# Performance work log

Measured on AMD Instinct MI355X. Metric: run time of the kernel, lower is better.

## Reference

```python
import jax, jax.numpy as jnp
import numpy as np

B, N, D, H, C = 4, 512, 128, 128, 3


def setup_inputs() -> dict:
    key = jax.random.key(0)
    k1, k2, k3, k4, k5 = jax.random.split(key, 5)
    s1 = 1.0 / np.sqrt(2 * D)  # torch Linear default init scale (uniform bound); randn is fine for a numerics baseline
    s2 = 1.0 / np.sqrt(H)
    return {
        "h_dense": jax.random.normal(k1, (B, N, D), dtype=jnp.float32),
        "W1": jax.random.normal(k2, (H, 2 * D), dtype=jnp.float32) * s1,
        "b1": jax.random.normal(k3, (H,), dtype=jnp.float32) * s1,
        "W2": jax.random.normal(k4, (C, H), dtype=jnp.float32) * s2,
        "b2": jax.random.normal(k5, (C,), dtype=jnp.float32) * s2,
    }


def reference(h_dense, W1, b1, W2, b2):
    # Linear(concat(h_src, h_dst)) == h_src @ W1[:, :D].T + h_dst @ W1[:, D:].T + b1
    # which avoids materializing the (B, N, N, 2D) concat tensor (same math).
    d = h_dense.shape[-1]
    a = jnp.einsum("bnd,hd->bnh", h_dense, W1[:, :d])  # src projection (B, N, H)
    b = jnp.einsum("bnd,hd->bnh", h_dense, W1[:, d:])  # dst projection (B, N, H)
    pre = a[:, :, None, :] + b[:, None, :, :] + b1      # (B, N, N, H)
    act = jax.nn.silu(pre)
    logits = jnp.einsum("bijh,ch->bijc", act, W2) + b2  # (B, N, N, C)
    # symmetrize over the pair axes (dropout is identity in eval mode)
    return (logits + jnp.swapaxes(logits, 1, 2)) * 0.5
```

## Files before the change

### kernel.cpp

```cpp
#include <hip/hip_runtime.h>
#include <hip/hip_fp16.h>

#define B_ 4
#define N_ 512
#define D_ 128
#define H_ 128
#define C_ 3

#define NEG_LOG2E   (-1.4426950408889634f)
#define NEG_HALF_LN2 (-0.34657359027997264f)
#define ROWP 136

typedef _Float16 half8  __attribute__((ext_vector_type(8)));
typedef _Float16 half4v __attribute__((ext_vector_type(4)));

__device__ __forceinline__ float exp2_fast(float x) {
    return __builtin_amdgcn_exp2f(x);
}

__global__ __launch_bounds__(256) void proj_gemm(
    const float* __restrict__ hd, const float* __restrict__ W1,
    const float* __restrict__ b1, _Float16* __restrict__ At, _Float16* __restrict__ Bt)
{
    __shared__ float hsT[64][36];
    __shared__ float wt [64][68];
    const int m0      = blockIdx.x * 32;
    const int by      = blockIdx.y;
    const int halfSel = by >> 1;
    const int wrow0   = (by & 1) * 64;

    const int t  = threadIdx.x;
    const int r  = t >> 4, c4 = t & 15;
    const int tx = t & 15, ty = t >> 4;

    float acc[2][4] = {};

    for (int kc = 0; kc < 2; ++kc) {
        if (kc) __syncthreads();
        #pragma unroll
        for (int i = 0; i < 2; ++i) {
            const int m = r + 16 * i;
            float4 v = *(const float4*)&hd[(m0 + m) * D_ + kc * 64 + 4 * c4];
            hsT[4 * c4 + 0][m] = v.x; hsT[4 * c4 + 1][m] = v.y;
            hsT[4 * c4 + 2][m] = v.z; hsT[4 * c4 + 3][m] = v.w;
        }
        #pragma unroll
        for (int i = 0; i < 4; ++i) {
            const int o = r + 16 * i;
            float4 v = *(const float4*)&W1[(wrow0 + o) * (2 * D_) + halfSel * D_ + kc * 64 + 4 * c4];
            wt[4 * c4 + 0][o] = v.x; wt[4 * c4 + 1][o] = v.y;
            wt[4 * c4 + 2][o] = v.z; wt[4 * c4 + 3][o] = v.w;
        }
        __syncthreads();
        #pragma unroll 8
        for (int k = 0; k < 64; ++k) {
            float2 a  = *(const float2*)&hsT[k][2 * ty];
            float4 bv = *(const float4*)&wt [k][4 * tx];
            acc[0][0] = fmaf(a.x, bv.x, acc[0][0]); acc[0][1] = fmaf(a.x, bv.y, acc[0][1]);
            acc[0][2] = fmaf(a.x, bv.z, acc[0][2]); acc[0][3] = fmaf(a.x, bv.w, acc[0][3]);
            acc[1][0] = fmaf(a.y, bv.x, acc[1][0]); acc[1][1] = fmaf(a.y, bv.y, acc[1][1]);
            acc[1][2] = fmaf(a.y, bv.z, acc[1][2]); acc[1][3] = fmaf(a.y, bv.w, acc[1][3]);
        }
    }

    _Float16* dst = halfSel ? Bt : At;
    const int ocol = wrow0 + 4 * tx;
    float4 bias = make_float4(0.f, 0.f, 0.f, 0.f);
    if (!halfSel) bias = *(const float4*)&b1[ocol];
    #pragma unroll
    for (int i = 0; i < 2; ++i) {
        half4v o;
        o[0] = (_Float16)((acc[i][0] + bias.x) * NEG_LOG2E);
        o[1] = (_Float16)((acc[i][1] + bias.y) * NEG_LOG2E);
        o[2] = (_Float16)((acc[i][2] + bias.z) * NEG_LOG2E);
        o[3] = (_Float16)((acc[i][3] + bias.w) * NEG_LOG2E);
        *(half4v*)&dst[(m0 + 2 * ty + i) * H_ + ocol] = o;
    }
}

__global__ __launch_bounds__(256, 8) void pair_kernel(
    const _Float16* __restrict__ At, const _Float16* __restrict__ Bt,
    const float* __restrict__ W2, const float* __restrict__ b2,
    float* __restrict__ out)
{
    __shared__ __align__(16) _Float16 AI[16 * ROWP], AJ[16 * ROWP];
    __shared__ __align__(16) _Float16 BI[16 * ROWP], BJ[16 * ROWP];
    const int T = N_ / 16;
    int tp = blockIdx.x;
    const int b = blockIdx.y;
    int I = 0;
    while (tp >= T - I) { tp -= T - I; ++I; }
    const int J = I + tp;

    const int tid = threadIdx.x;
    {
        const int r = tid >> 4, c = (tid & 15) * 8;
        const half8* sAI = (const half8*)(At + (b * N_ + I * 16) * H_);
        const half8* sAJ = (const half8*)(At + (b * N_ + J * 16) * H_);
        const half8* sBI = (const half8*)(Bt + (b * N_ + I * 16) * H_);
        const half8* sBJ = (const half8*)(Bt + (b * N_ + J * 16) * H_);
        *(half8*)&AI[r * ROWP + c] = sAI[tid];
        *(half8*)&AJ[r * ROWP + c] = sAJ[tid];
        *(half8*)&BI[r * ROWP + c] = sBI[tid];
        *(half8*)&BJ[r * ROWP + c] = sBJ[tid];
    }
    __syncthreads();

    const int ti = tid >> 4, tj = tid & 15;
    float acc0 = 0.f, acc1 = 0.f, acc2 = 0.f;

    #pragma unroll 4
    for (int h8 = 0; h8 < H_ / 8; ++h8) {
        const int hb = h8 * 8;
        half8 ai8 = *(const half8*)&AI[ti * ROWP + hb];
        half8 bj8 = *(const half8*)&BJ[tj * ROWP + hb];
        half8 aj8 = *(const half8*)&AJ[tj * ROWP + hb];
        half8 bi8 = *(const half8*)&BI[ti * ROWP + hb];
        float4 w0a = *(const float4*)&W2[hb],          w0b = *(const float4*)&W2[hb + 4];
        float4 w1a = *(const float4*)&W2[H_ + hb],     w1b = *(const float4*)&W2[H_ + hb + 4];
        float4 w2a = *(const float4*)&W2[2 * H_ + hb], w2b = *(const float4*)&W2[2 * H_ + hb + 4];
        const float w0[8] = {w0a.x, w0a.y, w0a.z, w0a.w, w0b.x, w0b.y, w0b.z, w0b.w};
        const float w1[8] = {w1a.x, w1a.y, w1a.z, w1a.w, w1b.x, w1b.y, w1b.z, w1b.w};
        const float w2[8] = {w2a.x, w2a.y, w2a.z, w2a.w, w2b.x, w2b.y, w2b.z, w2b.w};

        #pragma unroll
        for (int e = 0; e < 8; ++e) {
            const float y1 = (float)(ai8[e] + bj8[e]);
            const float y2 = (float)(aj8[e] + bi8[e]);
            const float d1 = 1.0f + exp2_fast(y1);
            const float d2 = 1.0f + exp2_fast(y2);
            const float rr = __builtin_amdgcn_rcpf(d1 * d2);
            const float s  = fmaf(y2, d1, y1 * d2) * rr;
            acc0 = fmaf(s, w0[e], acc0);
            acc1 = fmaf(s, w1[e], acc1);
            acc2 = fmaf(s, w2[e], acc2);
        }
    }

    const float o0 = fmaf(NEG_HALF_LN2, acc0, b2[0]);
    const float o1 = fmaf(NEG_HALF_LN2, acc1, b2[1]);
    const float o2 = fmaf(NEG_HALF_LN2, acc2, b2[2]);
    const int i = I * 16 + ti, j = J * 16 + tj;
    float* p1 = out + ((size_t)(b * N_ + i) * N_ + j) * C_;
    float* p2 = out + ((size_t)(b * N_ + j) * N_ + i) * C_;
    p1[0] = o0; p1[1] = o1; p1[2] = o2;
    p2[0] = o0; p2[1] = o1; p2[2] = o2;
}

extern "C" void kernel_launch(void* const* d_in, const int* in_sizes, int n_in,
                              void* d_out, int out_size, void* d_ws, size_t ws_size,
                              hipStream_t stream) {
    const float* hd = (const float*)d_in[0];
    const float* W1 = (const float*)d_in[1];
    const float* b1 = (const float*)d_in[2];
    const float* W2 = (const float*)d_in[3];
    const float* b2 = (const float*)d_in[4];
    float* out = (float*)d_out;

    _Float16* At = (_Float16*)d_ws;
    _Float16* Bt = At + B_ * N_ * H_;

    proj_gemm<<<dim3((B_ * N_) / 32, 4), dim3(256), 0, stream>>>(hd, W1, b1, At, Bt);

    const int T = N_ / 16;
    pair_kernel<<<dim3(T * (T + 1) / 2, B_), dim3(256), 0, stream>>>(At, Bt, W2, b2, out);
}
```

Before: 48.08 us.

## Precompute exp2 of projections and compute pair SiLU in packed fp16

The projection kernel now also writes exp2 of each projected value, so the pair kernel gets exp(a+b) as a product exp(a)*exp(b) instead of calling exp per pair element. The symmetric sigmoid numerator and denominator are computed in packed half2 arithmetic, leaving only a reciprocal per element in fp32. The pair kernel is reorganised into 64-thread blocks where each thread handles one j and four i rows, reading directly from global memory (no LDS staging) over a triangular tile enumeration. The workspace grows to four fp16 buffers, and fp16 products of exponentials risk overflow or precision loss for large inputs.

Result: slower. 62.24 us (+29.5%).

```diff
diff --git a/kernel.cpp b/kernel.cpp
--- a/kernel.cpp
+++ b/kernel.cpp
@@ -9,10 +9,10 @@
 
 #define NEG_LOG2E   (-1.4426950408889634f)
 #define NEG_HALF_LN2 (-0.34657359027997264f)
-#define ROWP 136
 
 typedef _Float16 half8  __attribute__((ext_vector_type(8)));
 typedef _Float16 half4v __attribute__((ext_vector_type(4)));
+typedef _Float16 half2v __attribute__((ext_vector_type(2)));
 
 __device__ __forceinline__ float exp2_fast(float x) {
     return __builtin_amdgcn_exp2f(x);
@@ -20,7 +20,9 @@
 
 __global__ __launch_bounds__(256) void proj_gemm(
     const float* __restrict__ hd, const float* __restrict__ W1,
-    const float* __restrict__ b1, _Float16* __restrict__ At, _Float16* __restrict__ Bt)
+    const float* __restrict__ b1,
+    _Float16* __restrict__ At,  _Float16* __restrict__ Bt,
+    _Float16* __restrict__ EAt, _Float16* __restrict__ EBt)
 {
     __shared__ float hsT[64][36];
     __shared__ float wt [64][68];
@@ -63,59 +65,61 @@
         }
     }
 
-    _Float16* dst = halfSel ? Bt : At;
+    _Float16* dst  = halfSel ? Bt  : At;
+    _Float16* edst = halfSel ? EBt : EAt;
     const int ocol = wrow0 + 4 * tx;
-    float4 bias = make_float4(0.f, 0.f, 0.f, 0.f);
-    if (!halfSel) bias = *(const float4*)&b1[ocol];
+    float biasv[4] = {0.f, 0.f, 0.f, 0.f};
+    if (!halfSel) {
+        float4 bb = *(const float4*)&b1[ocol];
+        biasv[0] = bb.x; biasv[1] = bb.y; biasv[2] = bb.z; biasv[3] = bb.w;
+    }
     #pragma unroll
     for (int i = 0; i < 2; ++i) {
-        half4v o;
-        o[0] = (_Float16)((acc[i][0] + bias.x) * NEG_LOG2E);
-        o[1] = (_Float16)((acc[i][1] + bias.y) * NEG_LOG2E);
-        o[2] = (_Float16)((acc[i][2] + bias.z) * NEG_LOG2E);
-        o[3] = (_Float16)((acc[i][3] + bias.w) * NEG_LOG2E);
-        *(half4v*)&dst[(m0 + 2 * ty + i) * H_ + ocol] = o;
+        half4v o, ee;
+        #pragma unroll
+        for (int k = 0; k < 4; ++k) {
+            o[k]  = (_Float16)((acc[i][k] + biasv[k]) * NEG_LOG2E);
+            ee[k] = (_Float16)exp2_fast((float)o[k]);
+        }
+        const size_t off = (size_t)(m0 + 2 * ty + i) * H_ + ocol;
+        *(half4v*)&dst[off]  = o;
+        *(half4v*)&edst[off] = ee;
     }
 }
 
-__global__ __launch_bounds__(256, 8) void pair_kernel(
-    const _Float16* __restrict__ At, const _Float16* __restrict__ Bt,
+__global__ __launch_bounds__(64, 4) void pair_kernel(
+    const _Float16* __restrict__ At,  const _Float16* __restrict__ Bt,
+    const _Float16* __restrict__ EAt, const _Float16* __restrict__ EBt,
     const float* __restrict__ W2, const float* __restrict__ b2,
     float* __restrict__ out)
 {
-    __shared__ __align__(16) _Float16 AI[16 * ROWP], AJ[16 * ROWP];
-    __shared__ __align__(16) _Float16 BI[16 * ROWP], BJ[16 * ROWP];
-    const int T = N_ / 16;
-    int tp = blockIdx.x;
     const int b = blockIdx.y;
-    int I = 0;
-    while (tp >= T - I) { tp -= T - I; ++I; }
-    const int J = I + tp;
+    int x = blockIdx.x;
+    int jt = 0;
+    for (;;) {
+        int cnt = 16 * (jt + 1); if (cnt > 128) cnt = 128;
+        if (x < cnt) break;
+        x -= cnt; ++jt;
+    }
+    const int i0 = x * 4;
+    const int j  = jt * 64 + (int)threadIdx.x;
 
-    const int tid = threadIdx.x;
-    {
-        const int r = tid >> 4, c = (tid & 15) * 8;
-        const half8* sAI = (const half8*)(At + (b * N_ + I * 16) * H_);
-        const half8* sAJ = (const half8*)(At + (b * N_ + J * 16) * H_);
-        const half8* sBI = (const half8*)(Bt + (b * N_ + I * 16) * H_);
-        const half8* sBJ = (const half8*)(Bt + (b * N_ + J * 16) * H_);
-        *(half8*)&AI[r * ROWP + c] = sAI[tid];
-        *(half8*)&AJ[r * ROWP + c] = sAJ[tid];
-        *(half8*)&BI[r * ROWP + c] = sBI[tid];
-        *(half8*)&BJ[r * ROWP + c] = sBJ[tid];
-    }
-    __syncthreads();
+    const size_t jbase = ((size_t)(b * N_) + j)  * H_;
+    const size_t ibase = ((size_t)(b * N_) + i0) * H_;
 
-    const int ti = tid >> 4, tj = tid & 15;
-    float acc0 = 0.f, acc1 = 0.f, acc2 = 0.f;
+    float acc[4][3] = {};
 
-    #pragma unroll 4
-    for (int h8 = 0; h8 < H_ / 8; ++h8) {
-        const int hb = h8 * 8;
-        half8 ai8 = *(const half8*)&AI[ti * ROWP + hb];
-        half8 bj8 = *(const half8*)&BJ[tj * ROWP + hb];
-        half8 aj8 = *(const half8*)&AJ[tj * ROWP + hb];
-        half8 bi8 = *(const half8*)&BI[ti * ROWP + hb];
+    for (int ch = 0; ch < 16; ++ch) {
+        const int hb = ch * 8;
+        const half8 yAj = *(const half8*)&At [jbase + hb];
+        const half8 yBj = *(const half8*)&Bt [jbase + hb];
+        const half8 eAj = *(const half8*)&EAt[jbase + hb];
+        const half8 eBj = *(const half8*)&EBt[jbase + hb];
+        const half2v* yAj2p = (const half2v*)&yAj;
+        const half2v* yBj2p = (const half2v*)&yBj;
+        const half2v* eAj2p = (const half2v*)&eAj;
+        const half2v* eBj2p = (const half2v*)&eBj;
+
         float4 w0a = *(const float4*)&W2[hb],          w0b = *(const float4*)&W2[hb + 4];
         float4 w1a = *(const float4*)&W2[H_ + hb],     w1b = *(const float4*)&W2[H_ + hb + 4];
         float4 w2a = *(const float4*)&W2[2 * H_ + hb], w2b = *(const float4*)&W2[2 * H_ + hb + 4];
@@ -124,27 +128,54 @@
         const float w2[8] = {w2a.x, w2a.y, w2a.z, w2a.w, w2b.x, w2b.y, w2b.z, w2b.w};
 
         #pragma unroll
-        for (int e = 0; e < 8; ++e) {
-            const float y1 = (float)(ai8[e] + bj8[e]);
-            const float y2 = (float)(aj8[e] + bi8[e]);
-            const float d1 = 1.0f + exp2_fast(y1);
-            const float d2 = 1.0f + exp2_fast(y2);
-            const float rr = __builtin_amdgcn_rcpf(d1 * d2);
-            const float s  = fmaf(y2, d1, y1 * d2) * rr;
-            acc0 = fmaf(s, w0[e], acc0);
-            acc1 = fmaf(s, w1[e], acc1);
-            acc2 = fmaf(s, w2[e], acc2);
+        for (int ii = 0; ii < 4; ++ii) {
+            const size_t ir = ibase + (size_t)ii * H_ + hb;
+            const half8 yAi = *(const half8*)&At [ir];
+            const half8 yBi = *(const half8*)&Bt [ir];
+            const half8 eAi = *(const half8*)&EAt[ir];
+            const half8 eBi = *(const half8*)&EBt[ir];
+            const half2v* yAi2p = (const half2v*)&yAi;
+            const half2v* yBi2p = (const half2v*)&yBi;
+            const half2v* eAi2p = (const half2v*)&eAi;
+            const half2v* eBi2p = (const half2v*)&eBi;
+
+            #pragma unroll
+            for (int q = 0; q < 4; ++q) {
+                half2v y1 = yAi2p[q] + yBj2p[q];
+                half2v y2 = yAj2p[q] + yBi2p[q];
+                half2v e1 = eAi2p[q] * eBj2p[q];
+                half2v e2 = eAj2p[q] * eBi2p[q];
+                half2v d1 = e1 + (_Float16)1.0f;
+                half2v d2 = e2 + (_Float16)1.0f;
+                half2v pp  = d1 * d2;
+                half2v num = y1 * d2 + y2 * d1;
+
+                #pragma unroll
+                for (int e = 0; e < 2; ++e) {
+                    const float s = (float)num[e] * __builtin_amdgcn_rcpf((float)pp[e]);
+                    const int hh = 2 * q + e;
+                    acc[ii][0] = fmaf(s, w0[hh], acc[ii][0]);
+                    acc[ii][1] = fmaf(s, w1[hh], acc[ii][1]);
+                    acc[ii][2] = fmaf(s, w2[hh], acc[ii][2]);
+                }
+            }
         }
     }
 
-    const float o0 = fmaf(NEG_HALF_LN2, acc0, b2[0]);
-    const float o1 = fmaf(NEG_HALF_LN2, acc1, b2[1]);
-    const float o2 = fmaf(NEG_HALF_LN2, acc2, b2[2]);
-    const int i = I * 16 + ti, j = J * 16 + tj;
-    float* p1 = out + ((size_t)(b * N_ + i) * N_ + j) * C_;
-    float* p2 = out + ((size_t)(b * N_ + j) * N_ + i) * C_;
-    p1[0] = o0; p1[1] = o1; p1[2] = o2;
-    p2[0] = o0; p2[1] = o1; p2[2] = o2;
+    const float b20 = b2[0], b21 = b2[1], b22 = b2[2];
+    #pragma unroll
+    for (int ii = 0; ii < 4; ++ii) {
+        const int i = i0 + ii;
+        if (j >= i) {
+            const float o0 = fmaf(NEG_HALF_LN2, acc[ii][0], b20);
+            const float o1 = fmaf(NEG_HALF_LN2, acc[ii][1], b21);
+            const float o2 = fmaf(NEG_HALF_LN2, acc[ii][2], b22);
+            float* p1 = out + ((size_t)(b * N_ + i) * N_ + j) * C_;
+            float* p2 = out + ((size_t)(b * N_ + j) * N_ + i) * C_;
+            p1[0] = o0; p1[1] = o1; p1[2] = o2;
+            p2[0] = o0; p2[1] = o1; p2[2] = o2;
+        }
+    }
 }
 
 extern "C" void kernel_launch(void* const* d_in, const int* in_sizes, int n_in,
@@ -157,11 +188,12 @@
     const float* b2 = (const float*)d_in[4];
     float* out = (float*)d_out;
 
-    _Float16* At = (_Float16*)d_ws;
-    _Float16* Bt = At + B_ * N_ * H_;
+    _Float16* At  = (_Float16*)d_ws;
+    _Float16* Bt  = At  + B_ * N_ * H_;
+    _Float16* EAt = Bt  + B_ * N_ * H_;
+    _Float16* EBt = EAt + B_ * N_ * H_;
 
-    proj_gemm<<<dim3((B_ * N_) / 32, 4), dim3(256), 0, stream>>>(hd, W1, b1, At, Bt);
+    proj_gemm<<<dim3((B_ * N_) / 32, 4), dim3(256), 0, stream>>>(hd, W1, b1, At, Bt, EAt, EBt);
 
-    const int T = N_ / 16;
-    pair_kernel<<<dim3(T * (T + 1) / 2, B_), dim3(256), 0, stream>>>(At, Bt, W2, b2, out);
+    pair_kernel<<<dim3(576, B_), dim3(64), 0, stream>>>(At, Bt, EAt, EBt, W2, b2, out);
 }
```

## Precompute exp2 of projections and factor pairwise exp into fp16 products

Applied to the files above, without the earlier changes.

The projection kernel now also writes exp2 of each projected value, so the pair kernel can form exp(a+b) as a product of two precomputed exponentials instead of calling exp2 per pair element. The sigmoid numerator and denominator are computed in packed fp16 vector arithmetic, and only one reciprocal per element stays in fp32. The pair kernel stages only the J tile in shared memory and reads the I-side rows directly from global memory, and its occupancy hint drops from 8 to 4 blocks. This doubles workspace traffic and risks fp16 overflow or precision loss in the exponential products.

New measurement: 57.12 us. +18.8%, slower.

```diff
diff --git a/kernel.cpp b/kernel.cpp
--- a/kernel.cpp
+++ b/kernel.cpp
@@ -9,7 +9,7 @@
 
 #define NEG_LOG2E   (-1.4426950408889634f)
 #define NEG_HALF_LN2 (-0.34657359027997264f)
-#define ROWP 136
+#define TPAD 132
 
 typedef _Float16 half8  __attribute__((ext_vector_type(8)));
 typedef _Float16 half4v __attribute__((ext_vector_type(4)));
@@ -20,7 +20,9 @@
 
 __global__ __launch_bounds__(256) void proj_gemm(
     const float* __restrict__ hd, const float* __restrict__ W1,
-    const float* __restrict__ b1, _Float16* __restrict__ At, _Float16* __restrict__ Bt)
+    const float* __restrict__ b1,
+    _Float16* __restrict__ At,  _Float16* __restrict__ Bt,
+    _Float16* __restrict__ EAt, _Float16* __restrict__ EBt)
 {
     __shared__ float hsT[64][36];
     __shared__ float wt [64][68];
@@ -63,59 +65,82 @@
         }
     }
 
-    _Float16* dst = halfSel ? Bt : At;
+    _Float16* dst  = halfSel ? Bt  : At;
+    _Float16* edst = halfSel ? EBt : EAt;
     const int ocol = wrow0 + 4 * tx;
-    float4 bias = make_float4(0.f, 0.f, 0.f, 0.f);
-    if (!halfSel) bias = *(const float4*)&b1[ocol];
+    float biasv[4] = {0.f, 0.f, 0.f, 0.f};
+    if (!halfSel) {
+        float4 bb = *(const float4*)&b1[ocol];
+        biasv[0] = bb.x; biasv[1] = bb.y; biasv[2] = bb.z; biasv[3] = bb.w;
+    }
     #pragma unroll
     for (int i = 0; i < 2; ++i) {
-        half4v o;
-        o[0] = (_Float16)((acc[i][0] + bias.x) * NEG_LOG2E);
-        o[1] = (_Float16)((acc[i][1] + bias.y) * NEG_LOG2E);
-        o[2] = (_Float16)((acc[i][2] + bias.z) * NEG_LOG2E);
-        o[3] = (_Float16)((acc[i][3] + bias.w) * NEG_LOG2E);
-        *(half4v*)&dst[(m0 + 2 * ty + i) * H_ + ocol] = o;
+        half4v o, ee;
+        #pragma unroll
+        for (int k = 0; k < 4; ++k) {
+            o[k]  = (_Float16)((acc[i][k] + biasv[k]) * NEG_LOG2E);
+            ee[k] = (_Float16)exp2_fast((float)o[k]);
+        }
+        const size_t off = (size_t)(m0 + 2 * ty + i) * H_ + ocol;
+        *(half4v*)&dst[off]  = o;
+        *(half4v*)&edst[off] = ee;
     }
 }
 
-__global__ __launch_bounds__(256, 8) void pair_kernel(
-    const _Float16* __restrict__ At, const _Float16* __restrict__ Bt,
+__global__ __launch_bounds__(256, 4) void pair_kernel(
+    const _Float16* __restrict__ At,  const _Float16* __restrict__ Bt,
+    const _Float16* __restrict__ EAt, const _Float16* __restrict__ EBt,
     const float* __restrict__ W2, const float* __restrict__ b2,
     float* __restrict__ out)
 {
-    __shared__ __align__(16) _Float16 AI[16 * ROWP], AJ[16 * ROWP];
-    __shared__ __align__(16) _Float16 BI[16 * ROWP], BJ[16 * ROWP];
-    const int T = N_ / 16;
+    __shared__ __align__(16) _Float16 jt[4][16 * TPAD];
+    const int b = blockIdx.y;
     int tp = blockIdx.x;
-    const int b = blockIdx.y;
     int I = 0;
-    while (tp >= T - I) { tp -= T - I; ++I; }
+    while (tp >= 32 - I) { tp -= 32 - I; ++I; }
     const int J = I + tp;
 
     const int tid = threadIdx.x;
-    {
-        const int r = tid >> 4, c = (tid & 15) * 8;
-        const half8* sAI = (const half8*)(At + (b * N_ + I * 16) * H_);
-        const half8* sAJ = (const half8*)(At + (b * N_ + J * 16) * H_);
-        const half8* sBI = (const half8*)(Bt + (b * N_ + I * 16) * H_);
-        const half8* sBJ = (const half8*)(Bt + (b * N_ + J * 16) * H_);
-        *(half8*)&AI[r * ROWP + c] = sAI[tid];
-        *(half8*)&AJ[r * ROWP + c] = sAJ[tid];
-        *(half8*)&BI[r * ROWP + c] = sBI[tid];
-        *(half8*)&BJ[r * ROWP + c] = sBJ[tid];
+    #pragma unroll
+    for (int k = 0; k < 4; ++k) {
+        const int u   = tid + 256 * k;
+        const int tl  = u >> 8;
+        const int row = (u >> 4) & 15;
+        const int c   = u & 15;
+        const _Float16* src = (tl == 0) ? At : (tl == 1) ? Bt : (tl == 2) ? EAt : EBt;
+        half8 v = *(const half8*)&src[((size_t)(b * N_) + J * 16 + row) * H_ + c * 8];
+        *(half8*)&jt[tl][row * TPAD + c * 8] = v;
     }
     __syncthreads();
 
     const int ti = tid >> 4, tj = tid & 15;
+    const int i = I * 16 + ti, j = J * 16 + tj;
+    const size_t ibase = ((size_t)(b * N_) + i) * H_;
+
     float acc0 = 0.f, acc1 = 0.f, acc2 = 0.f;
 
     #pragma unroll 4
-    for (int h8 = 0; h8 < H_ / 8; ++h8) {
-        const int hb = h8 * 8;
-        half8 ai8 = *(const half8*)&AI[ti * ROWP + hb];
-        half8 bj8 = *(const half8*)&BJ[tj * ROWP + hb];
-        half8 aj8 = *(const half8*)&AJ[tj * ROWP + hb];
-        half8 bi8 = *(const half8*)&BI[ti * ROWP + hb];
+    for (int ch = 0; ch < 16; ++ch) {
+        const int hb = ch * 8;
+        const half8 yAi = *(const half8*)&At [ibase + hb];
+        const half8 yBi = *(const half8*)&Bt [ibase + hb];
+        const half8 eAi = *(const half8*)&EAt[ibase + hb];
+        const half8 eBi = *(const half8*)&EBt[ibase + hb];
+        const int jo = tj * TPAD + hb;
+        const half8 yAj = *(const half8*)&jt[0][jo];
+        const half8 yBj = *(const half8*)&jt[1][jo];
+        const half8 eAj = *(const half8*)&jt[2][jo];
+        const half8 eBj = *(const half8*)&jt[3][jo];
+
+        half8 y1 = yAi + yBj;
+        half8 y2 = yAj + yBi;
+        half8 e1 = eAi * eBj;
+        half8 e2 = eAj * eBi;
+        half8 d1 = e1 + (_Float16)1.0f;
+        half8 d2 = e2 + (_Float16)1.0f;
+        half8 pp  = d1 * d2;
+        half8 num = y1 * d2 + y2 * d1;
+
         float4 w0a = *(const float4*)&W2[hb],          w0b = *(const float4*)&W2[hb + 4];
         float4 w1a = *(const float4*)&W2[H_ + hb],     w1b = *(const float4*)&W2[H_ + hb + 4];
         float4 w2a = *(const float4*)&W2[2 * H_ + hb], w2b = *(const float4*)&W2[2 * H_ + hb + 4];
@@ -125,12 +150,7 @@
 
         #pragma unroll
         for (int e = 0; e < 8; ++e) {
-            const float y1 = (float)(ai8[e] + bj8[e]);
-            const float y2 = (float)(aj8[e] + bi8[e]);
-            const float d1 = 1.0f + exp2_fast(y1);
-            const float d2 = 1.0f + exp2_fast(y2);
-            const float rr = __builtin_amdgcn_rcpf(d1 * d2);
-            const float s  = fmaf(y2, d1, y1 * d2) * rr;
+            const float s = (float)num[e] * __builtin_amdgcn_rcpf((float)pp[e]);
             acc0 = fmaf(s, w0[e], acc0);
             acc1 = fmaf(s, w1[e], acc1);
             acc2 = fmaf(s, w2[e], acc2);
@@ -140,7 +160,6 @@
     const float o0 = fmaf(NEG_HALF_LN2, acc0, b2[0]);
     const float o1 = fmaf(NEG_HALF_LN2, acc1, b2[1]);
     const float o2 = fmaf(NEG_HALF_LN2, acc2, b2[2]);
-    const int i = I * 16 + ti, j = J * 16 + tj;
     float* p1 = out + ((size_t)(b * N_ + i) * N_ + j) * C_;
     float* p2 = out + ((size_t)(b * N_ + j) * N_ + i) * C_;
     p1[0] = o0; p1[1] = o1; p1[2] = o2;
@@ -157,11 +176,12 @@
     const float* b2 = (const float*)d_in[4];
     float* out = (float*)d_out;
 
-    _Float16* At = (_Float16*)d_ws;
-    _Float16* Bt = At + B_ * N_ * H_;
+    _Float16* At  = (_Float16*)d_ws;
+    _Float16* Bt  = At  + B_ * N_ * H_;
+    _Float16* EAt = Bt  + B_ * N_ * H_;
+    _Float16* EBt = EAt + B_ * N_ * H_;
 
-    proj_gemm<<<dim3((B_ * N_) / 32, 4), dim3(256), 0, stream>>>(hd, W1, b1, At, Bt);
+    proj_gemm<<<dim3((B_ * N_) / 32, 4), dim3(256), 0, stream>>>(hd, W1, b1, At, Bt, EAt, EBt);
 
-    const int T = N_ / 16;
-    pair_kernel<<<dim3(T * (T + 1) / 2, B_), dim3(256), 0, stream>>>(At, Bt, W2, b2, out);
+    pair_kernel<<<dim3(528, B_), dim3(256), 0, stream>>>(At, Bt, EAt, EBt, W2, b2, out);
 }
```
